# Kernel tuning notes

Measured on AMD Instinct MI355X. Metric: run time of the kernel, lower is better.

Reference implementation:

```python
import jax, jax.numpy as jnp
import numpy as np
import math

D_MODEL = 1024
N_HEAD = 16
D_HEAD = D_MODEL // N_HEAD  # 64
D_KMAP = 128
B, L = 4, 4096


def setup_inputs() -> dict:
    key = jax.random.key(0)
    ks = jax.random.split(key, 10)
    s = 1.0 / math.sqrt(D_MODEL)
    inp = {
        "x": jax.random.normal(ks[0], (B, L, D_MODEL), dtype=jnp.float32),
        "proj_mat": jax.random.normal(ks[1], (D_HEAD, D_KMAP), dtype=jnp.float32),
        "Wq": jax.random.uniform(ks[2], (D_MODEL, D_MODEL), minval=-s, maxval=s),
        "bq": jax.random.uniform(ks[3], (D_MODEL,), minval=-s, maxval=s),
        "Wk": jax.random.uniform(ks[4], (D_MODEL, D_MODEL), minval=-s, maxval=s),
        "bk": jax.random.uniform(ks[5], (D_MODEL,), minval=-s, maxval=s),
        "Wv": jax.random.uniform(ks[6], (D_MODEL, D_MODEL), minval=-s, maxval=s),
        "bv": jax.random.uniform(ks[7], (D_MODEL,), minval=-s, maxval=s),
        "Wo": jax.random.uniform(ks[8], (D_MODEL, D_MODEL), minval=-s, maxval=s),
        "bo": jax.random.uniform(ks[9], (D_MODEL,), minval=-s, maxval=s),
    }
    return inp


def _fourier_kernel(x, proj_mat):
    # x: [B,L,H,d_head] -> [B,L,H,2*d_kmap]
    p = jnp.einsum("blhd,dm->blhm", x, proj_mat) / math.sqrt(D_HEAD)
    return jnp.concatenate([jnp.cos(p), jnp.sin(p)], axis=-1) / math.sqrt(D_KMAP)


def reference(x, proj_mat, Wq, bq, Wk, bk, Wv, bv, Wo, bo):
    Bv, Lv, _ = x.shape
    q = (x @ Wq.T + bq).reshape(Bv, Lv, N_HEAD, D_HEAD)
    k = (x @ Wk.T + bk).reshape(Bv, Lv, N_HEAD, D_HEAD)
    v = (x @ Wv.T + bv).reshape(Bv, Lv, N_HEAD, D_HEAD)
    q_prime = _fourier_kernel(q, proj_mat)  # [B,L,H,2M]
    k_prime = _fourier_kernel(k, proj_mat)  # [B,L,H,2M]
    kv = jnp.einsum("blhm,blhd->bhmd", k_prime, v)  # [B,H,2M,d_head]
    out = jnp.einsum("blhm,bhmd->blhd", q_prime, kv)  # [B,L,H,d_head]
    out = out.reshape(Bv, Lv, D_MODEL)
    return out @ Wo.T + bo
```

## Files before the change

### kernel.cpp

```cpp
#include <hip/hip_runtime.h>
#include <cstddef>
#include <cstdint>


typedef __attribute__((ext_vector_type(8))) short s8v;
typedef __attribute__((ext_vector_type(4))) short s4v;
typedef __attribute__((ext_vector_type(4))) float f32x4;

#define MFMA_BF16(a, b, c) __builtin_amdgcn_mfma_f32_16x16x32_bf16((a), (b), (c), 0, 0, 0)

#define P_SCALE 0.125f
#define F_SCALE 0.08838834764831845f

static __device__ __forceinline__ unsigned short f2bf(float f) {
  unsigned int u = __float_as_uint(f);
  u += 0x7fffu + ((u >> 16) & 1u);
  return (unsigned short)(u >> 16);
}

static __device__ __forceinline__ void gload_lds16(const void* g, void* l) {
  __builtin_amdgcn_global_load_lds(
      (const __attribute__((address_space(1))) unsigned int*)g,
      (__attribute__((address_space(3))) unsigned int*)l, 16, 0, 0);
}

__global__ void conv_all_kernel(const float* __restrict__ x,
                                const float* __restrict__ Wq, const float* __restrict__ Wk,
                                const float* __restrict__ Wv, const float* __restrict__ Wo,
                                const float* __restrict__ proj,
                                short* __restrict__ xb, short* __restrict__ Wqkvb,
                                short* __restrict__ Wob, short* __restrict__ projT) {
  const int T = blockIdx.x * 256 + threadIdx.x;
  for (int u = T; u < 5244928; u += 524288) {
    if (u < 4194304) {
      float4 f = ((const float4*)x)[u];
      s4v v;
      v[0] = (short)f2bf(f.x); v[1] = (short)f2bf(f.y);
      v[2] = (short)f2bf(f.z); v[3] = (short)f2bf(f.w);
      ((s4v*)xb)[u] = v;
    } else if (u < 5242880) {
      int vi = u - 4194304;
      int wi = vi >> 18;
      int off = vi & 262143;
      const float* src = (wi == 0) ? Wq : (wi == 1) ? Wk : (wi == 2) ? Wv : Wo;
      short* dst = (wi < 3) ? (Wqkvb + (size_t)wi * 1048576) : Wob;
      float4 f = ((const float4*)src)[off];
      s4v v;
      v[0] = (short)f2bf(f.x); v[1] = (short)f2bf(f.y);
      v[2] = (short)f2bf(f.z); v[3] = (short)f2bf(f.w);
      ((s4v*)dst)[off] = v;
    } else {
      int vi = u - 5242880;
      int d = vi >> 5, m4 = (vi & 31) * 4;
      float4 f = ((const float4*)proj)[vi];
      projT[(m4 + 0) * 64 + d] = (short)f2bf(f.x);
      projT[(m4 + 1) * 64 + d] = (short)f2bf(f.y);
      projT[(m4 + 2) * 64 + d] = (short)f2bf(f.z);
      projT[(m4 + 3) * 64 + d] = (short)f2bf(f.w);
    }
  }
}

__global__ void qkv_gemm_kernel(const short* __restrict__ xb,
                                const short* __restrict__ Wqkv,
                                const float* __restrict__ bq_, const float* __restrict__ bk_,
                                const float* __restrict__ bv_,
                                short* __restrict__ qb, short* __restrict__ kb,
                                short* __restrict__ vT) {
  __shared__ __align__(16) short smem[17408];
  short* Al = smem;
  short* Bl = smem + 8192;

  const int t = threadIdx.x;
  const int bm = blockIdx.x, bn = blockIdx.y;
  const int row0 = bm * 128, n0 = bn * 128;
  const int lane = t & 63, w = t >> 6;
  const int wm = w & 1, wn = w >> 1;
  const int l15 = lane & 15, lq = lane >> 4;
  const int sx = (l15 & 7) * 8;

  f32x4 acc[4][4];
#pragma unroll
  for (int i = 0; i < 4; ++i)
#pragma unroll
    for (int j = 0; j < 4; ++j) acc[i][j] = (f32x4){0.f, 0.f, 0.f, 0.f};

  for (int k0 = 0; k0 < 1024; k0 += 64) {
#pragma unroll
    for (int i = 0; i < 4; ++i) {
      int c = t + i * 256;
      int r = c >> 3, cl = c & 7;
      int cg = cl ^ (r & 7);
      gload_lds16(xb   + (size_t)(row0 + r) * 1024 + k0 + cg * 8, Al + c * 8);
      gload_lds16(Wqkv + (size_t)(n0 + r) * 1024 + k0 + cg * 8, Bl + c * 8);
    }
    __syncthreads();
#pragma unroll
    for (int ks = 0; ks < 2; ++ks) {
      const int kb8 = (ks * 4 + lq) * 8;
      s8v af[4], bfr[4];
#pragma unroll
      for (int i = 0; i < 4; ++i)
        af[i] = *(s8v*)&Al[(wm * 64 + i * 16 + l15) * 64 + (kb8 ^ sx)];
#pragma unroll
      for (int j = 0; j < 4; ++j)
        bfr[j] = *(s8v*)&Bl[(wn * 64 + j * 16 + l15) * 64 + (kb8 ^ sx)];
#pragma unroll
      for (int i = 0; i < 4; ++i)
#pragma unroll
        for (int j = 0; j < 4; ++j)
          acc[i][j] = MFMA_BF16(af[i], bfr[j], acc[i][j]);
    }
    __syncthreads();
  }

  const int region = bn >> 3;
  if (region < 2) {
    const float* bias = (region == 0) ? bq_ : bk_;
    short* IM = smem;
#pragma unroll
    for (int j = 0; j < 4; ++j) {
      int cl = wn * 64 + j * 16 + l15;
      float bsv = bias[(n0 & 1023) + cl];
#pragma unroll
      for (int i = 0; i < 4; ++i)
#pragma unroll
        for (int r = 0; r < 4; ++r)
          IM[(wm * 64 + i * 16 + lq * 4 + r) * 136 + cl] = (short)f2bf(acc[i][j][r] + bsv);
    }
    __syncthreads();
    short* dst = (region == 0) ? qb : kb;
#pragma unroll
    for (int i = 0; i < 8; ++i) {
      int c = t + i * 256;
      int r = c >> 4, cc = c & 15;
      *(s8v*)&dst[(size_t)(row0 + r) * 1024 + (n0 & 1023) + cc * 8] =
          *(s8v*)&IM[r * 136 + cc * 8];
    }
  } else {
    short* IM = smem;
#pragma unroll
    for (int j = 0; j < 4; ++j) {
      int cl = wn * 64 + j * 16 + l15;
      float bsv = bv_[(n0 - 2048) + cl];
#pragma unroll
      for (int i = 0; i < 4; ++i) {
        s4v pk;
#pragma unroll
        for (int r = 0; r < 4; ++r) pk[r] = (short)f2bf(acc[i][j][r] + bsv);
        *(s4v*)&IM[cl * 136 + wm * 64 + i * 16 + lq * 4] = pk;
      }
    }
    __syncthreads();
    const int b = row0 >> 12;
    const int l0 = (bm & 31) * 128;
#pragma unroll
    for (int i = 0; i < 8; ++i) {
      int c = t + i * 256;
      int ci = c >> 4, cc = c & 15;
      int cv = (bn - 16) * 128 + ci;
      int grow = (b * 16 + (cv >> 6)) * 64 + (cv & 63);
      *(s8v*)&vT[(size_t)grow * 4096 + l0 + cc * 8] = *(s8v*)&IM[ci * 136 + cc * 8];
    }
  }
}

__global__ void kv_accum_kernel(const short* __restrict__ kb, const short* __restrict__ vT,
                                const short* __restrict__ projT, float* __restrict__ kv) {
  __shared__ __align__(16) short smem[26624];
  short* kt = smem;
  short* vt = smem + 4096;
  short* kpT = smem + 8192;

  const int t = threadIdx.x;
  const int bid = blockIdx.x;
  const int chunk = bid & 7, h = (bid >> 3) & 15, b = bid >> 7;
  const int lane = t & 63, w = t >> 6;
  const int l15 = lane & 15, lq = lane >> 4;
  const int sx = (l15 & 7) * 8;

  s8v pf[8][2];
#pragma unroll
  for (int nt = 0; nt < 8; ++nt)
#pragma unroll
    for (int ks = 0; ks < 2; ++ks)
      pf[nt][ks] = *(const s8v*)(projT + (size_t)(nt * 16 + l15) * 64 + ks * 32 + lq * 8);

  f32x4 kvacc[4][4];
#pragma unroll
  for (int i = 0; i < 4; ++i)
#pragma unroll
    for (int j = 0; j < 4; ++j) kvacc[i][j] = (f32x4){0.f, 0.f, 0.f, 0.f};

  for (int s = 0; s < 8; ++s) {
    const int l0s = chunk * 512 + s * 64;
#pragma unroll
    for (int i = 0; i < 2; ++i) {
      int c = t + i * 256;
      int r = c >> 3, cl = c & 7;
      int cg = cl ^ (r & 7);
      gload_lds16(kb + (size_t)(b * 4096 + l0s + r) * 1024 + h * 64 + cg * 8, kt + c * 8);
      gload_lds16(vT + (size_t)((b * 16 + h) * 64 + r) * 4096 + l0s + cg * 8, vt + c * 8);
    }
    __syncthreads();

    f32x4 pacc[8];
#pragma unroll
    for (int nt = 0; nt < 8; ++nt) pacc[nt] = (f32x4){0.f, 0.f, 0.f, 0.f};
#pragma unroll
    for (int ks = 0; ks < 2; ++ks) {
      const int kb8 = (ks * 4 + lq) * 8;
      s8v af = *(s8v*)&kt[(w * 16 + l15) * 64 + (kb8 ^ sx)];
#pragma unroll
      for (int nt = 0; nt < 8; ++nt) pacc[nt] = MFMA_BF16(af, pf[nt][ks], pacc[nt]);
    }
#pragma unroll
    for (int nt = 0; nt < 8; ++nt) {
      s4v cp, sp;
#pragma unroll
      for (int r = 0; r < 4; ++r) {
        float pv = pacc[nt][r] * P_SCALE;
        float sv, cv;
        __sincosf(pv, &sv, &cv);
        cp[r] = (short)f2bf(cv * F_SCALE);
        sp[r] = (short)f2bf(sv * F_SCALE);
      }
      int m = nt * 16 + l15;
      int rbase = w * 16 + lq * 4;
      *(s4v*)&kpT[m * 72 + rbase] = cp;
      *(s4v*)&kpT[(m + 128) * 72 + rbase] = sp;
    }
    __syncthreads();

#pragma unroll
    for (int ks = 0; ks < 2; ++ks) {
      const int kb8 = (ks * 4 + lq) * 8;
      s8v af[4], bf4[4];
#pragma unroll
      for (int i = 0; i < 4; ++i)
        af[i] = *(s8v*)&kpT[(w * 64 + i * 16 + l15) * 72 + ks * 32 + lq * 8];
#pragma unroll
      for (int j = 0; j < 4; ++j)
        bf4[j] = *(s8v*)&vt[(j * 16 + l15) * 64 + (kb8 ^ sx)];
#pragma unroll
      for (int i = 0; i < 4; ++i)
#pragma unroll
        for (int j = 0; j < 4; ++j)
          kvacc[i][j] = MFMA_BF16(af[i], bf4[j], kvacc[i][j]);
    }
    __syncthreads();
  }

  float* kvb = kv + (size_t)chunk * 1048576 + ((size_t)(b * 16 + h) << 14);
#pragma unroll
  for (int i = 0; i < 4; ++i)
#pragma unroll
    for (int j = 0; j < 4; ++j)
#pragma unroll
      for (int r = 0; r < 4; ++r) {
        int m = w * 64 + i * 16 + lq * 4 + r;
        int d = j * 16 + l15;
        kvb[(size_t)m * 64 + d] = kvacc[i][j][r];
      }
}

__global__ void kvT_kernel(const float* __restrict__ kvp, short* __restrict__ kvT) {
  __shared__ __align__(16) short im[4608];
  const int t = threadIdx.x;
  const int bh = blockIdx.x, mc = blockIdx.y;
  const float* base = kvp + (size_t)bh * 16384 + (size_t)mc * 4096;
#pragma unroll
  for (int i = 0; i < 4; ++i) {
    int idx4 = t + i * 256;
    int mm = idx4 >> 4, d4 = (idx4 & 15) * 4;
    float4 s = {0.f, 0.f, 0.f, 0.f};
#pragma unroll
    for (int c = 0; c < 8; ++c) {
      float4 v = *(const float4*)(base + (size_t)c * 1048576 + mm * 64 + d4);
      s.x += v.x; s.y += v.y; s.z += v.z; s.w += v.w;
    }
    im[(d4 + 0) * 72 + mm] = (short)f2bf(s.x);
    im[(d4 + 1) * 72 + mm] = (short)f2bf(s.y);
    im[(d4 + 2) * 72 + mm] = (short)f2bf(s.z);
    im[(d4 + 3) * 72 + mm] = (short)f2bf(s.w);
  }
  __syncthreads();
#pragma unroll
  for (int i = 0; i < 2; ++i) {
    int c = t + i * 256;
    int d = c >> 3, mm8 = (c & 7) * 8;
    *(s8v*)&kvT[(size_t)(bh * 64 + d) * 256 + mc * 64 + mm8] = *(s8v*)&im[d * 72 + mm8];
  }
}

__global__ void attn_kernel(const short* __restrict__ qb, const short* __restrict__ projT,
                            const short* __restrict__ kvT, short* __restrict__ attnb) {
  __shared__ __align__(16) short smem[20992];
  short* qt = smem;
  short* qA = smem + 4096;
  short* kvt = smem + 12800;

  const int t = threadIdx.x;
  const int rt = blockIdx.x, h = blockIdx.y;
  const int row0 = rt * 64;
  const int b = row0 >> 12;
  const int lane = t & 63, w = t >> 6;
  const int l15 = lane & 15, lq = lane >> 4;
  const int sx = (l15 & 7) * 8;

  s8v pf[8][2];
#pragma unroll
  for (int nt = 0; nt < 8; ++nt)
#pragma unroll
    for (int ks = 0; ks < 2; ++ks)
      pf[nt][ks] = *(const s8v*)(projT + (size_t)(nt * 16 + l15) * 64 + ks * 32 + lq * 8);

#pragma unroll
  for (int i = 0; i < 2; ++i) {
    int c = t + i * 256;
    int r = c >> 3, cl = c & 7;
    int cg = cl ^ (r & 7);
    gload_lds16(qb + (size_t)(row0 + r) * 1024 + h * 64 + cg * 8, qt + c * 8);
  }
  __syncthreads();

  f32x4 pacc[8];
#pragma unroll
  for (int nt = 0; nt < 8; ++nt) pacc[nt] = (f32x4){0.f, 0.f, 0.f, 0.f};
#pragma unroll
  for (int ks = 0; ks < 2; ++ks) {
    const int kb8 = (ks * 4 + lq) * 8;
    s8v af = *(s8v*)&qt[(w * 16 + l15) * 64 + (kb8 ^ sx)];
#pragma unroll
    for (int nt = 0; nt < 8; ++nt) pacc[nt] = MFMA_BF16(af, pf[nt][ks], pacc[nt]);
  }

  f32x4 aacc[4];
#pragma unroll
  for (int j = 0; j < 4; ++j) aacc[j] = (f32x4){0.f, 0.f, 0.f, 0.f};

#pragma unroll
  for (int half = 0; half < 2; ++half) {
#pragma unroll
    for (int nt = 0; nt < 8; ++nt)
#pragma unroll
      for (int r = 0; r < 4; ++r) {
        float p = pacc[nt][r] * P_SCALE;
        float fv = (half == 0) ? __cosf(p) : __sinf(p);
        qA[(w * 16 + lq * 4 + r) * 136 + nt * 16 + l15] = (short)f2bf(fv * F_SCALE);
      }
#pragma unroll
    for (int i = 0; i < 4; ++i) {
      int c = t + i * 256;
      int d = c >> 4, cl = c & 15;
      int cg = cl ^ (d & 15);
      gload_lds16(kvT + (size_t)((b * 16 + h) * 64 + d) * 256 + half * 128 + cg * 8,
                  kvt + c * 8);
    }
    __syncthreads();
#pragma unroll
    for (int ks = 0; ks < 4; ++ks) {
      s8v af = *(s8v*)&qA[(w * 16 + l15) * 136 + ks * 32 + lq * 8];
#pragma unroll
      for (int j = 0; j < 4; ++j) {
        int row = j * 16 + l15;
        s8v bf4 = *(s8v*)&kvt[row * 128 + (((ks * 4 + lq) ^ l15) * 8)];
        aacc[j] = MFMA_BF16(af, bf4, aacc[j]);
      }
    }
    __syncthreads();
  }

#pragma unroll
  for (int j = 0; j < 4; ++j)
#pragma unroll
    for (int r = 0; r < 4; ++r)
      smem[(w * 16 + lq * 4 + r) * 72 + j * 16 + l15] = (short)f2bf(aacc[j][r]);
  __syncthreads();
#pragma unroll
  for (int i = 0; i < 2; ++i) {
    int c = t + i * 256;
    int r = c >> 3, cc = c & 7;
    *(s8v*)&attnb[(size_t)(row0 + r) * 1024 + h * 64 + cc * 8] = *(s8v*)&smem[r * 72 + cc * 8];
  }
}

__global__ void out_gemm_kernel(const short* __restrict__ attnb, const short* __restrict__ Wob,
                                const float* __restrict__ bo_, float* __restrict__ out) {
  __shared__ __align__(16) short smem[16384];
  short* Al = smem;
  short* Bl = smem + 8192;

  const int t = threadIdx.x;
  const int bm = blockIdx.x, bn = blockIdx.y;
  const int row0 = bm * 128, n0 = bn * 128;
  const int lane = t & 63, w = t >> 6;
  const int wm = w & 1, wn = w >> 1;
  const int l15 = lane & 15, lq = lane >> 4;
  const int sx = (l15 & 7) * 8;

  f32x4 acc[4][4];
#pragma unroll
  for (int i = 0; i < 4; ++i)
#pragma unroll
    for (int j = 0; j < 4; ++j) acc[i][j] = (f32x4){0.f, 0.f, 0.f, 0.f};

  for (int k0 = 0; k0 < 1024; k0 += 64) {
#pragma unroll
    for (int i = 0; i < 4; ++i) {
      int c = t + i * 256;
      int r = c >> 3, cl = c & 7;
      int cg = cl ^ (r & 7);
      gload_lds16(attnb + (size_t)(row0 + r) * 1024 + k0 + cg * 8, Al + c * 8);
      gload_lds16(Wob   + (size_t)(n0 + r) * 1024 + k0 + cg * 8, Bl + c * 8);
    }
    __syncthreads();
#pragma unroll
    for (int ks = 0; ks < 2; ++ks) {
      const int kb8 = (ks * 4 + lq) * 8;
      s8v af[4], bfr[4];
#pragma unroll
      for (int i = 0; i < 4; ++i)
        af[i] = *(s8v*)&Al[(wm * 64 + i * 16 + l15) * 64 + (kb8 ^ sx)];
#pragma unroll
      for (int j = 0; j < 4; ++j)
        bfr[j] = *(s8v*)&Bl[(wn * 64 + j * 16 + l15) * 64 + (kb8 ^ sx)];
#pragma unroll
      for (int i = 0; i < 4; ++i)
#pragma unroll
        for (int j = 0; j < 4; ++j)
          acc[i][j] = MFMA_BF16(af[i], bfr[j], acc[i][j]);
    }
    __syncthreads();
  }

#pragma unroll
  for (int j = 0; j < 4; ++j) {
    int cl = wn * 64 + j * 16 + l15;
    float bsv = bo_[n0 + cl];
#pragma unroll
    for (int i = 0; i < 4; ++i)
#pragma unroll
      for (int r = 0; r < 4; ++r)
        out[(size_t)(row0 + wm * 64 + i * 16 + lq * 4 + r) * 1024 + n0 + cl] =
            acc[i][j][r] + bsv;
  }
}

extern "C" void kernel_launch(void* const* d_in, const int* in_sizes, int n_in,
                              void* d_out, int out_size, void* d_ws, size_t ws_size,
                              hipStream_t stream) {
  const float* x    = (const float*)d_in[0];
  const float* proj = (const float*)d_in[1];
  const float* Wq   = (const float*)d_in[2];
  const float* bq   = (const float*)d_in[3];
  const float* Wk   = (const float*)d_in[4];
  const float* bk   = (const float*)d_in[5];
  const float* Wv   = (const float*)d_in[6];
  const float* bv   = (const float*)d_in[7];
  const float* Wo   = (const float*)d_in[8];
  const float* bo   = (const float*)d_in[9];
  float* out = (float*)d_out;

  char* wsb = (char*)d_ws;
  short* qb    = (short*)(wsb + 0);
  short* kb    = (short*)(wsb + 33554432);
  short* vT    = (short*)(wsb + 67108864);
  short* xb    = (short*)(wsb + 100663296);
  short* Wqkvb = (short*)(wsb + 134217728);
  short* Wob   = (short*)(wsb + 140509184);
  short* projT = (short*)(wsb + 142606336);
  float* kv_part = (float*)(wsb + 100663296);
  short* attnb = kb;
  short* kvT   = vT;

  conv_all_kernel<<<dim3(2048), dim3(256), 0, stream>>>(
      x, Wq, Wk, Wv, Wo, proj, xb, Wqkvb, Wob, projT);

  qkv_gemm_kernel<<<dim3(128, 24), dim3(256), 0, stream>>>(xb, Wqkvb, bq, bk, bv, qb, kb, vT);
  kv_accum_kernel<<<dim3(512), dim3(256), 0, stream>>>(kb, vT, projT, kv_part);
  kvT_kernel<<<dim3(64, 4), dim3(256), 0, stream>>>(kv_part, kvT);
  attn_kernel<<<dim3(256, 16), dim3(256), 0, stream>>>(qb, projT, kvT, attnb);
  out_gemm_kernel<<<dim3(128, 8), dim3(256), 0, stream>>>(attnb, Wob, bo, out);
}
```

Measured before the change: 393.3 us.

## Double-buffer K/V loads in kv_accum and prefetch both kvT halves in attn

In kv_accum_kernel, the K and V tiles are now double-buffered in LDS. The next tile's async global->LDS load is issued before computing on the current one, and explicit vmcnt waits with raw barriers replace __syncthreads. The kpT staging buffer also moves from a padded layout to an XOR-swizzled 64-wide layout to cut bank conflicts while saving space. In attn_kernel, both halves of kvT are prefetched up front together with q, and partial vmcnt waits let the cosine half start while the sine half is still loading. The cost is more LDS per block, which may lower occupancy, and reliance on hand-tuned waitcnt counts that must match the issued loads.

```diff
diff --git a/kernel.cpp b/kernel.cpp
--- a/kernel.cpp
+++ b/kernel.cpp
@@ -23,6 +23,10 @@
       (const __attribute__((address_space(1))) unsigned int*)g,
       (__attribute__((address_space(3))) unsigned int*)l, 16, 0, 0);
 }
+
+#define VMC(n) asm volatile("s_waitcnt vmcnt(" #n ")" ::: "memory")
+#define LGKM0 asm volatile("s_waitcnt lgkmcnt(0)" ::: "memory")
+#define RBAR  { __builtin_amdgcn_s_barrier(); __builtin_amdgcn_sched_barrier(0); }
 
 __global__ void conv_all_kernel(const float* __restrict__ x,
                                 const float* __restrict__ Wq, const float* __restrict__ Wk,
@@ -167,10 +171,10 @@
 
 __global__ void kv_accum_kernel(const short* __restrict__ kb, const short* __restrict__ vT,
                                 const short* __restrict__ projT, float* __restrict__ kv) {
-  __shared__ __align__(16) short smem[26624];
+  __shared__ __align__(16) short smem[32768];
   short* kt = smem;
-  short* vt = smem + 4096;
-  short* kpT = smem + 8192;
+  short* vt = smem + 8192;
+  short* kpT = smem + 16384;
 
   const int t = threadIdx.x;
   const int bid = blockIdx.x;
@@ -192,17 +196,21 @@
 #pragma unroll
     for (int j = 0; j < 4; ++j) kvacc[i][j] = (f32x4){0.f, 0.f, 0.f, 0.f};
 
+#define STAGE_KV(pp, ss) {                                                       \
+    const int l0s = chunk * 512 + (ss) * 64;                                     \
+    _Pragma("unroll") for (int i = 0; i < 2; ++i) {                              \
+      int c = t + i * 256; int r = c >> 3, cl = c & 7, cg = cl ^ (r & 7);        \
+      gload_lds16(kb + (size_t)(b * 4096 + l0s + r) * 1024 + h * 64 + cg * 8,    \
+                  kt + (pp) * 4096 + c * 8);                                     \
+      gload_lds16(vT + (size_t)((b * 16 + h) * 64 + r) * 4096 + l0s + cg * 8,    \
+                  vt + (pp) * 4096 + c * 8);                                     \
+    } }
+
+  int p = 0;
+  STAGE_KV(0, 0);
   for (int s = 0; s < 8; ++s) {
-    const int l0s = chunk * 512 + s * 64;
-#pragma unroll
-    for (int i = 0; i < 2; ++i) {
-      int c = t + i * 256;
-      int r = c >> 3, cl = c & 7;
-      int cg = cl ^ (r & 7);
-      gload_lds16(kb + (size_t)(b * 4096 + l0s + r) * 1024 + h * 64 + cg * 8, kt + c * 8);
-      gload_lds16(vT + (size_t)((b * 16 + h) * 64 + r) * 4096 + l0s + cg * 8, vt + c * 8);
-    }
-    __syncthreads();
+    if (s < 7) { STAGE_KV(p ^ 1, s + 1); VMC(4); } else { VMC(0); }
+    RBAR;
 
     f32x4 pacc[8];
 #pragma unroll
@@ -210,46 +218,54 @@
 #pragma unroll
     for (int ks = 0; ks < 2; ++ks) {
       const int kb8 = (ks * 4 + lq) * 8;
-      s8v af = *(s8v*)&kt[(w * 16 + l15) * 64 + (kb8 ^ sx)];
+      s8v af = *(s8v*)&kt[p * 4096 + (w * 16 + l15) * 64 + (kb8 ^ sx)];
 #pragma unroll
       for (int nt = 0; nt < 8; ++nt) pacc[nt] = MFMA_BF16(af, pf[nt][ks], pacc[nt]);
     }
-#pragma unroll
-    for (int nt = 0; nt < 8; ++nt) {
-      s4v cp, sp;
-#pragma unroll
-      for (int r = 0; r < 4; ++r) {
-        float pv = pacc[nt][r] * P_SCALE;
-        float sv, cv;
-        __sincosf(pv, &sv, &cv);
-        cp[r] = (short)f2bf(cv * F_SCALE);
-        sp[r] = (short)f2bf(sv * F_SCALE);
+    {
+      const int cidx = w * 2 + (lq >> 1);
+      const int within = (lq & 1) * 4;
+#pragma unroll
+      for (int nt = 0; nt < 8; ++nt) {
+        s4v cp, sp;
+#pragma unroll
+        for (int r = 0; r < 4; ++r) {
+          float pv = pacc[nt][r] * P_SCALE;
+          float sv, cv;
+          __sincosf(pv, &sv, &cv);
+          cp[r] = (short)f2bf(cv * F_SCALE);
+          sp[r] = (short)f2bf(sv * F_SCALE);
+        }
+        int m = nt * 16 + l15;
+        int col = ((cidx ^ (m & 7)) << 3) + within;
+        *(s4v*)&kpT[m * 64 + col] = cp;
+        *(s4v*)&kpT[(m + 128) * 64 + col] = sp;
       }
-      int m = nt * 16 + l15;
-      int rbase = w * 16 + lq * 4;
-      *(s4v*)&kpT[m * 72 + rbase] = cp;
-      *(s4v*)&kpT[(m + 128) * 72 + rbase] = sp;
-    }
-    __syncthreads();
+    }
+    LGKM0;
+    RBAR;
 
 #pragma unroll
     for (int ks = 0; ks < 2; ++ks) {
       const int kb8 = (ks * 4 + lq) * 8;
-      s8v af[4], bf4[4];
-#pragma unroll
-      for (int i = 0; i < 4; ++i)
-        af[i] = *(s8v*)&kpT[(w * 64 + i * 16 + l15) * 72 + ks * 32 + lq * 8];
+      s8v af2[4], bf4[4];
+#pragma unroll
+      for (int i = 0; i < 4; ++i)
+        af2[i] = *(s8v*)&kpT[(w * 64 + i * 16 + l15) * 64 +
+                             (((ks * 4 + lq) ^ (l15 & 7)) * 8)];
 #pragma unroll
       for (int j = 0; j < 4; ++j)
-        bf4[j] = *(s8v*)&vt[(j * 16 + l15) * 64 + (kb8 ^ sx)];
+        bf4[j] = *(s8v*)&vt[p * 4096 + (j * 16 + l15) * 64 + (kb8 ^ sx)];
 #pragma unroll
       for (int i = 0; i < 4; ++i)
 #pragma unroll
         for (int j = 0; j < 4; ++j)
-          kvacc[i][j] = MFMA_BF16(af[i], bf4[j], kvacc[i][j]);
-    }
-    __syncthreads();
-  }
+          kvacc[i][j] = MFMA_BF16(af2[i], bf4[j], kvacc[i][j]);
+    }
+    RBAR;
+    p ^= 1;
+  }
+#undef STAGE_KV
 
   float* kvb = kv + (size_t)chunk * 1048576 + ((size_t)(b * 16 + h) << 14);
 #pragma unroll
@@ -295,7 +311,7 @@
 
 __global__ void attn_kernel(const short* __restrict__ qb, const short* __restrict__ projT,
                             const short* __restrict__ kvT, short* __restrict__ attnb) {
-  __shared__ __align__(16) short smem[20992];
+  __shared__ __align__(16) short smem[29184];
   short* qt = smem;
   short* qA = smem + 4096;
   short* kvt = smem + 12800;
@@ -322,7 +338,18 @@
     int cg = cl ^ (r & 7);
     gload_lds16(qb + (size_t)(row0 + r) * 1024 + h * 64 + cg * 8, qt + c * 8);
   }
-  __syncthreads();
+#pragma unroll
+  for (int half = 0; half < 2; ++half)
+#pragma unroll
+    for (int i = 0; i < 4; ++i) {
+      int c = t + i * 256;
+      int d = c >> 4, cl = c & 15;
+      int cg = cl ^ (d & 15);
+      gload_lds16(kvT + (size_t)((b * 16 + h) * 64 + d) * 256 + half * 128 + cg * 8,
+                  kvt + half * 8192 + c * 8);
+    }
+  VMC(8);
+  RBAR;
 
   f32x4 pacc[8];
 #pragma unroll
@@ -349,28 +376,21 @@
         float fv = (half == 0) ? __cosf(p) : __sinf(p);
         qA[(w * 16 + lq * 4 + r) * 136 + nt * 16 + l15] = (short)f2bf(fv * F_SCALE);
       }
-#pragma unroll
-    for (int i = 0; i < 4; ++i) {
-      int c = t + i * 256;
-      int d = c >> 4, cl = c & 15;
-      int cg = cl ^ (d & 15);
-      gload_lds16(kvT + (size_t)((b * 16 + h) * 64 + d) * 256 + half * 128 + cg * 8,
-                  kvt + c * 8);
-    }
-    __syncthreads();
+    if (half == 0) { VMC(4); } else { VMC(0); }
+    RBAR;
 #pragma unroll
     for (int ks = 0; ks < 4; ++ks) {
       s8v af = *(s8v*)&qA[(w * 16 + l15) * 136 + ks * 32 + lq * 8];
 #pragma unroll
       for (int j = 0; j < 4; ++j) {
         int row = j * 16 + l15;
-        s8v bf4 = *(s8v*)&kvt[row * 128 + (((ks * 4 + lq) ^ l15) * 8)];
+        s8v bf4 = *(s8v*)&kvt[half * 8192 + row * 128 + (((ks * 4 + lq) ^ l15) * 8)];
         aacc[j] = MFMA_BF16(af, bf4, aacc[j]);
       }
     }
-    __syncthreads();
-  }
-
+  }
+
+  __syncthreads();
 #pragma unroll
   for (int j = 0; j < 4; ++j)
 #pragma unroll
```

After: 402.5 us. 2.3% more time.

## Enlarge attn blocks to 128 rows and prefetch both kv halves up front

Applied to the files above, without the earlier changes.

The attention kernel now uses 512-thread blocks covering 128 rows, so each kv tile load into shared memory is shared by twice as many rows. Q fragments are read straight from global memory into registers instead of staging through LDS. Both kv halves are issued as async global-to-LDS loads at kernel start, and the per-half waits use vmcnt counters with raw barriers so the second half's load overlaps the first half's compute. This trades higher LDS use per block (possibly lower occupancy) for fewer barriers and less redundant kv traffic.

```diff
diff --git a/kernel.cpp b/kernel.cpp
--- a/kernel.cpp
+++ b/kernel.cpp
@@ -23,6 +23,10 @@
       (const __attribute__((address_space(1))) unsigned int*)g,
       (__attribute__((address_space(3))) unsigned int*)l, 16, 0, 0);
 }
+
+#define VMC(n) asm volatile("s_waitcnt vmcnt(" #n ")" ::: "memory")
+#define LGKM0 asm volatile("s_waitcnt lgkmcnt(0)" ::: "memory")
+#define RBAR  { __builtin_amdgcn_s_barrier(); __builtin_amdgcn_sched_barrier(0); }
 
 __global__ void conv_all_kernel(const float* __restrict__ x,
                                 const float* __restrict__ Wq, const float* __restrict__ Wk,
@@ -295,18 +299,16 @@
 
 __global__ void attn_kernel(const short* __restrict__ qb, const short* __restrict__ projT,
                             const short* __restrict__ kvT, short* __restrict__ attnb) {
-  __shared__ __align__(16) short smem[20992];
-  short* qt = smem;
-  short* qA = smem + 4096;
-  short* kvt = smem + 12800;
+  __shared__ __align__(16) short smem[33792];
+  short* qA = smem;
+  short* kvt = smem + 17408;
 
   const int t = threadIdx.x;
   const int rt = blockIdx.x, h = blockIdx.y;
-  const int row0 = rt * 64;
+  const int row0 = rt * 128;
   const int b = row0 >> 12;
   const int lane = t & 63, w = t >> 6;
   const int l15 = lane & 15, lq = lane >> 4;
-  const int sx = (l15 & 7) * 8;
 
   s8v pf[8][2];
 #pragma unroll
@@ -315,25 +317,30 @@
     for (int ks = 0; ks < 2; ++ks)
       pf[nt][ks] = *(const s8v*)(projT + (size_t)(nt * 16 + l15) * 64 + ks * 32 + lq * 8);
 
-#pragma unroll
-  for (int i = 0; i < 2; ++i) {
-    int c = t + i * 256;
-    int r = c >> 3, cl = c & 7;
-    int cg = cl ^ (r & 7);
-    gload_lds16(qb + (size_t)(row0 + r) * 1024 + h * 64 + cg * 8, qt + c * 8);
-  }
-  __syncthreads();
+  s8v qf[2];
+#pragma unroll
+  for (int ks = 0; ks < 2; ++ks)
+    qf[ks] = *(const s8v*)&qb[(size_t)(row0 + w * 16 + l15) * 1024 + h * 64 +
+                              (ks * 4 + lq) * 8];
+
+#pragma unroll
+  for (int half = 0; half < 2; ++half)
+#pragma unroll
+    for (int i = 0; i < 2; ++i) {
+      int c = t + i * 512;
+      int d = c >> 4, cl = c & 15;
+      int cg = cl ^ (d & 15);
+      gload_lds16(kvT + (size_t)((b * 16 + h) * 64 + d) * 256 + half * 128 + cg * 8,
+                  kvt + half * 8192 + c * 8);
+    }
 
   f32x4 pacc[8];
 #pragma unroll
   for (int nt = 0; nt < 8; ++nt) pacc[nt] = (f32x4){0.f, 0.f, 0.f, 0.f};
 #pragma unroll
-  for (int ks = 0; ks < 2; ++ks) {
-    const int kb8 = (ks * 4 + lq) * 8;
-    s8v af = *(s8v*)&qt[(w * 16 + l15) * 64 + (kb8 ^ sx)];
-#pragma unroll
-    for (int nt = 0; nt < 8; ++nt) pacc[nt] = MFMA_BF16(af, pf[nt][ks], pacc[nt]);
-  }
+  for (int ks = 0; ks < 2; ++ks)
+#pragma unroll
+    for (int nt = 0; nt < 8; ++nt) pacc[nt] = MFMA_BF16(qf[ks], pf[nt][ks], pacc[nt]);
 
   f32x4 aacc[4];
 #pragma unroll
@@ -349,26 +356,20 @@
         float fv = (half == 0) ? __cosf(p) : __sinf(p);
         qA[(w * 16 + lq * 4 + r) * 136 + nt * 16 + l15] = (short)f2bf(fv * F_SCALE);
       }
-#pragma unroll
-    for (int i = 0; i < 4; ++i) {
-      int c = t + i * 256;
-      int d = c >> 4, cl = c & 15;
-      int cg = cl ^ (d & 15);
-      gload_lds16(kvT + (size_t)((b * 16 + h) * 64 + d) * 256 + half * 128 + cg * 8,
-                  kvt + c * 8);
-    }
-    __syncthreads();
+    LGKM0;
+    if (half == 0) { VMC(2); } else { VMC(0); }
+    RBAR;
 #pragma unroll
     for (int ks = 0; ks < 4; ++ks) {
       s8v af = *(s8v*)&qA[(w * 16 + l15) * 136 + ks * 32 + lq * 8];
 #pragma unroll
       for (int j = 0; j < 4; ++j) {
         int row = j * 16 + l15;
-        s8v bf4 = *(s8v*)&kvt[row * 128 + (((ks * 4 + lq) ^ l15) * 8)];
+        s8v bf4 = *(s8v*)&kvt[half * 8192 + row * 128 + (((ks * 4 + lq) ^ l15) * 8)];
         aacc[j] = MFMA_BF16(af, bf4, aacc[j]);
       }
     }
-    __syncthreads();
+    if (half == 0) RBAR;
   }
 
 #pragma unroll
@@ -379,7 +380,7 @@
   __syncthreads();
 #pragma unroll
   for (int i = 0; i < 2; ++i) {
-    int c = t + i * 256;
+    int c = t + i * 512;
     int r = c >> 3, cc = c & 7;
     *(s8v*)&attnb[(size_t)(row0 + r) * 1024 + h * 64 + cc * 8] = *(s8v*)&smem[r * 72 + cc * 8];
   }
@@ -480,6 +481,6 @@
   qkv_gemm_kernel<<<dim3(128, 24), dim3(256), 0, stream>>>(xb, Wqkvb, bq, bk, bv, qb, kb, vT);
   kv_accum_kernel<<<dim3(512), dim3(256), 0, stream>>>(kb, vT, projT, kv_part);
   kvT_kernel<<<dim3(64, 4), dim3(256), 0, stream>>>(kv_part, kvT);
-  attn_kernel<<<dim3(256, 16), dim3(256), 0, stream>>>(qb, projT, kvT, attnb);
+  attn_kernel<<<dim3(128, 16), dim3(512), 0, stream>>>(qb, projT, kvT, attnb);
   out_gemm_kernel<<<dim3(128, 8), dim3(256), 0, stream>>>(attnb, Wob, bo, out);
 }
```

After: 398.1 us. Within noise of the previous version (+1.2%).
